# Performance work log

Hardware: AMD Instinct MI355X
Metric: run time of the kernel (lower is better)

The kernel has to match this reference:

```python
import jax, jax.numpy as jnp
import numpy as np

B, S, DIM = 2, 2048, 2048
N_HEADS, N_KV_HEADS = 16, 4
HEAD_DIM = DIM // N_HEADS  # 128
N_REP = N_HEADS // N_KV_HEADS  # 4
ROPE_THETA = 10000.0


def setup_inputs() -> dict:
    key = jax.random.key(0)
    ks = jax.random.split(key, 6)
    x = jax.random.normal(ks[0], (B, S, DIM), dtype=jnp.float32)
    # torch nn.Linear weights are [out_features, in_features]
    sc = 0.02
    wq = jax.random.normal(ks[1], (N_HEADS * HEAD_DIM, DIM), dtype=jnp.float32) * sc
    wk = jax.random.normal(ks[2], (N_KV_HEADS * HEAD_DIM, DIM), dtype=jnp.float32) * sc
    wv = jax.random.normal(ks[3], (N_KV_HEADS * HEAD_DIM, DIM), dtype=jnp.float32) * sc
    wo = jax.random.normal(ks[4], (DIM, N_HEADS * HEAD_DIM), dtype=jnp.float32) * sc
    # precomputed rotary table (freqs_cis in llama): [S, head_dim//2]
    inv_freq = 1.0 / (ROPE_THETA ** (jnp.arange(0, HEAD_DIM, 2, dtype=jnp.float32) / HEAD_DIM))
    t = jnp.arange(S, dtype=jnp.float32)
    freqs = jnp.outer(t, inv_freq)  # [S, head_dim//2]
    freqs_cos = jnp.cos(freqs)
    freqs_sin = jnp.sin(freqs)
    # additive causal mask as passed to SDPA (float, 0 on allowed, -inf-like elsewhere)
    causal = jnp.tril(jnp.ones((S, S), dtype=bool))
    mask = jnp.where(causal, 0.0, -1e9).astype(jnp.float32)
    return {"x": x, "wq": wq, "wk": wk, "wv": wv, "wo": wo,
            "freqs_cos": freqs_cos, "freqs_sin": freqs_sin, "mask": mask}


def _apply_rope(t, cos, sin):
    # t: [B, S, H, D]; cos/sin: [S, D//2] -> complex multiply on adjacent pairs
    tr = t.reshape(*t.shape[:-1], -1, 2)  # [B,S,H,D/2,2]
    tre, tim = tr[..., 0], tr[..., 1]
    c = cos[None, :, None, :]
    s = sin[None, :, None, :]
    out_re = tre * c - tim * s
    out_im = tre * s + tim * c
    return jnp.stack([out_re, out_im], axis=-1).reshape(t.shape)


def reference(x, wq, wk, wv, wo, freqs_cos, freqs_sin, mask):
    Bx, Sx, _ = x.shape
    xq = (x @ wq.T).reshape(Bx, Sx, N_HEADS, HEAD_DIM)
    xk = (x @ wk.T).reshape(Bx, Sx, N_KV_HEADS, HEAD_DIM)
    xv = (x @ wv.T).reshape(Bx, Sx, N_KV_HEADS, HEAD_DIM)
    xq = _apply_rope(xq, freqs_cos, freqs_sin)
    xk = _apply_rope(xk, freqs_cos, freqs_sin)
    # repeat_kv for GQA: [B,S,KV,D] -> [B,S,KV*n_rep,D]
    keys = jnp.repeat(xk, N_REP, axis=2)
    values = jnp.repeat(xv, N_REP, axis=2)
    q = xq.transpose(0, 2, 1, 3)      # [B,H,S,D]
    k = keys.transpose(0, 2, 1, 3)
    v = values.transpose(0, 2, 1, 3)
    scale = 1.0 / jnp.sqrt(jnp.float32(HEAD_DIM))
    scores = jnp.einsum('bhqd,bhkd->bhqk', q, k) * scale + mask[None, None]
    attn = jax.nn.softmax(scores, axis=-1)
    out = jnp.einsum('bhqk,bhkd->bhqd', attn, v)
    out = out.transpose(0, 2, 1, 3).reshape(Bx, Sx, -1)
    return out @ wo.T
```

## Files before the change

kernel.cpp:

```cpp
#include <hip/hip_runtime.h>
#include <hip/hip_bf16.h>

#define B_   2
#define S_   2048
#define DIM_ 2048
#define NH   16
#define NKV  4
#define HD   128
#define QKVN 3072

typedef __attribute__((ext_vector_type(8)))  short  sv8;
typedef __attribute__((ext_vector_type(8)))  ushort usv8;
typedef __attribute__((ext_vector_type(4)))  float  fv4;
typedef __attribute__((ext_vector_type(16))) float  fv16;

__device__ __forceinline__ float fast_exp2(float x) {
  return __builtin_amdgcn_exp2f(x);
}

__device__ __forceinline__ ushort f2bf(float f) {
  __hip_bfloat16 h = __float2bfloat16(f);
  union { __hip_bfloat16 h; ushort u; } c; c.h = h; return c.u;
}
__device__ __forceinline__ float bf2f(ushort u) {
  union { unsigned int i; float f; } c; c.i = ((unsigned)u) << 16; return c.f;
}

__device__ __forceinline__ unsigned int cvtpk(float lo, float hi) {
  unsigned int r;
  asm("v_cvt_pk_bf16_f32 %0, %1, %2" : "=v"(r) : "v"(lo), "v"(hi));
  return r;
}
__device__ __forceinline__ unsigned int xhalf(unsigned int x) {
  return (unsigned int)__shfl_xor((int)x, 32, 64);
}

__device__ __forceinline__ float tmax16(const fv16& v) {
  float a = fmaxf(fmaxf(v[0], v[1]),  fmaxf(v[2], v[3]));
  float b = fmaxf(fmaxf(v[4], v[5]),  fmaxf(v[6], v[7]));
  float c = fmaxf(fmaxf(v[8], v[9]),  fmaxf(v[10], v[11]));
  float d = fmaxf(fmaxf(v[12], v[13]), fmaxf(v[14], v[15]));
  return fmaxf(fmaxf(a, b), fmaxf(c, d));
}
__device__ __forceinline__ float tsum16(const fv16& v) {
  float a = (v[0] + v[1]) + (v[2] + v[3]);
  float b = (v[4] + v[5]) + (v[6] + v[7]);
  float c = (v[8] + v[9]) + (v[10] + v[11]);
  float d = (v[12] + v[13]) + (v[14] + v[15]);
  return (a + b) + (c + d);
}

__device__ __forceinline__ void async16(const void* g, void* l) {
  __builtin_amdgcn_global_load_lds(
      (const __attribute__((address_space(1))) unsigned int*)g,
      (__attribute__((address_space(3))) unsigned int*)l, 16, 0, 0);
}

__global__ void cvtall_kernel(const float* __restrict__ x,
                              const float* __restrict__ wq, const float* __restrict__ wk,
                              const float* __restrict__ wv, const float* __restrict__ wo,
                              const float* __restrict__ fc, const float* __restrict__ fs,
                              ushort* __restrict__ xb,
                              ushort* __restrict__ wqkvb, ushort* __restrict__ wob,
                              float* __restrict__ cs2) {
  const int NX = 2 * 2048 * 2048;
  const int NQ = 2048 * 2048, NK = 512 * 2048;
  const int CVT = NX + 2 * NQ + 2 * NK;
  int i = (blockIdx.x * 256 + threadIdx.x) * 4;
  if (i < CVT) {
    const float* src; ushort* dst;
    if (i < NX) { src = x + i; dst = xb + i; }
    else {
      int j = i - NX;
      if (j < NQ)               { src = wq + j;             dst = wqkvb + j; }
      else if (j < NQ + NK)     { src = wk + (j - NQ);      dst = wqkvb + j; }
      else if (j < NQ + 2 * NK) { src = wv + (j - NQ - NK); dst = wqkvb + j; }
      else                      { int k = j - (NQ + 2 * NK); src = wo + k; dst = wob + k; }
    }
    fv4 v = *(const fv4*)src;
    ushort4 o;
    o.x = f2bf(v[0]); o.y = f2bf(v[1]); o.z = f2bf(v[2]); o.w = f2bf(v[3]);
    *(ushort4*)dst = o;
  } else {
    int j = i - CVT;
    fv4 c = *(const fv4*)(fc + j);
    fv4 s = *(const fv4*)(fs + j);
    fv4 lo, hi;
    lo[0] = c[0]; lo[1] = s[0]; lo[2] = c[1]; lo[3] = s[1];
    hi[0] = c[2]; hi[1] = s[2]; hi[2] = c[3]; hi[3] = s[3];
    *(fv4*)(cs2 + 2 * j)     = lo;
    *(fv4*)(cs2 + 2 * j + 4) = hi;
  }
}

__global__ __launch_bounds__(256) void vtrans_kernel(const ushort* __restrict__ vraw,
                                                     ushort* __restrict__ vt, int rowstride) {
  __shared__ ushort tile[128][136];
  int blk = blockIdx.x;
  int st  = blk & 15;
  int kvb = blk >> 4;
  int kv  = kvb & 3;
  int b   = kvb >> 2;
  int s0  = st << 7;
#pragma unroll
  for (int it = 0; it < 8; ++it) {
    int t = it * 256 + threadIdx.x;
    int srow = t >> 4;
    int d8 = (t & 15) * 8;
    usv8 v = *(const usv8*)(vraw + (size_t)(b * S_ + s0 + srow) * rowstride + kv * HD + d8);
#pragma unroll
    for (int j = 0; j < 8; ++j) tile[d8 + j][srow] = v[j];
  }
  __syncthreads();
#pragma unroll
  for (int it = 0; it < 8; ++it) {
    int t = it * 256 + threadIdx.x;
    int d = t >> 4;
    int s8 = (t & 15) * 8;
    usv8 o;
#pragma unroll
    for (int j = 0; j < 8; ++j) o[j] = tile[d][s8 + j];
    *(usv8*)(vt + ((size_t)(b * NKV + kv) * HD + d) * S_ + s0 + s8) = o;
  }
}

__global__ __launch_bounds__(512) void gemm192_rope(const ushort* __restrict__ A,
                                                    const ushort* __restrict__ Bm,
                                                    const float* __restrict__ cs2,
                                                    ushort* __restrict__ qr,
                                                    ushort* __restrict__ kr,
                                                    ushort* __restrict__ Cv,
                                                    float qscale,
                                                    int M, int N, int K) {
  __shared__ __align__(16) ushort SM[57344];
  int nb = N / 192;
  int bx = blockIdx.x % nb, by = blockIdx.x / nb;
  int m0 = by << 8;
  int n0 = bx * 192;
  int tid = threadIdx.x;
  int lane = tid & 63, w = tid >> 6;
  int l15 = lane & 15, lg = lane >> 4;
  int wm = (w >> 2) * 128;
  int wn = (w & 3) * 48;
  int pA = w >> 2;

  int srow = tid >> 3;
  int cb   = ((tid & 7) * 16) ^ ((srow & 7) << 4);
  const ushort* sA = A  + (size_t)(m0 + srow) * K + (cb >> 1);
  const ushort* sB = Bm + (size_t)(n0 + srow) * K + (cb >> 1);
  size_t rstep = (size_t)64 * K;
  int nkt = K >> 6;

  auto STG_A = [&](int t, int db) {
    ushort* base = SM + db * 28672 + (w << 9);
    const ushort* a0 = sA + (size_t)t * 64;
    async16(a0,             base);
    async16(a0 + rstep,     base + 4096);
    async16(a0 + 2 * rstep, base + 8192);
    async16(a0 + 3 * rstep, base + 12288);
  };
  auto STG_B = [&](int t, int db) {
    ushort* base = SM + db * 28672 + 16384 + (w << 9);
    const ushort* b0 = sB + (size_t)t * 64;
    async16(b0,             base);
    async16(b0 + rstep,     base + 4096);
    async16(b0 + 2 * rstep, base + 8192);
  };

  fv4 acc[8][3] = {};
  sv8 alo[4][2], ahi[4][2], b01[2][2], b2v[2];

  STG_A(0, 0); STG_B(0, 0);
  { int t1 = nkt > 1 ? 1 : 0; STG_A(t1, 1); STG_B(t1, 1); }
  asm volatile("s_waitcnt vmcnt(7)");
  __builtin_amdgcn_s_barrier();

  for (int t = 0; t < nkt; ++t) {
    int db = t & 1;
    int t2 = t + 2 < nkt ? t + 2 : nkt - 1;
    const char* Ab = (const char*)(SM + db * 28672) + pA * 16384;
    const char* Bb = (const char*)(SM + db * 28672) + 32768;

#pragma unroll
    for (int m = 0; m < 4; ++m)
#pragma unroll
      for (int kk = 0; kk < 2; ++kk) {
        int row = m * 16 + l15;
        alo[m][kk] = *(const sv8*)(Ab + row * 128 + ((kk * 64 + lg * 16) ^ ((row & 7) << 4)));
      }
#pragma unroll
    for (int j = 0; j < 2; ++j)
#pragma unroll
      for (int kk = 0; kk < 2; ++kk) {
        int row = wn + j * 16 + l15;
        b01[j][kk] = *(const sv8*)(Bb + row * 128 + ((kk * 64 + lg * 16) ^ ((row & 7) << 4)));
      }
    __builtin_amdgcn_s_barrier();
    asm volatile("s_waitcnt lgkmcnt(0)");
    __builtin_amdgcn_s_setprio(1);
#pragma unroll
    for (int m = 0; m < 4; ++m)
#pragma unroll
      for (int j = 0; j < 2; ++j)
#pragma unroll
        for (int kk = 0; kk < 2; ++kk)
          acc[m][j] = __builtin_amdgcn_mfma_f32_16x16x32_bf16(alo[m][kk], b01[j][kk], acc[m][j], 0, 0, 0);
    __builtin_amdgcn_s_setprio(0);
    __builtin_amdgcn_s_barrier();

#pragma unroll
    for (int m = 0; m < 4; ++m)
#pragma unroll
      for (int kk = 0; kk < 2; ++kk) {
        int row = 64 + m * 16 + l15;
        ahi[m][kk] = *(const sv8*)(Ab + row * 128 + ((kk * 64 + lg * 16) ^ ((row & 7) << 4)));
      }
#pragma unroll
    for (int kk = 0; kk < 2; ++kk) {
      int row = wn + 32 + l15;
      b2v[kk] = *(const sv8*)(Bb + row * 128 + ((kk * 64 + lg * 16) ^ ((row & 7) << 4)));
    }
    __builtin_amdgcn_s_barrier();
    asm volatile("s_waitcnt lgkmcnt(0)");
    __builtin_amdgcn_s_setprio(1);
#pragma unroll
    for (int m = 0; m < 4; ++m)
#pragma unroll
      for (int kk = 0; kk < 2; ++kk)
        acc[m][2] = __builtin_amdgcn_mfma_f32_16x16x32_bf16(alo[m][kk], b2v[kk], acc[m][2], 0, 0, 0);
    __builtin_amdgcn_s_setprio(0);
    __builtin_amdgcn_s_barrier();

    STG_A(t2, db);
    __builtin_amdgcn_s_barrier();
    __builtin_amdgcn_s_setprio(1);
#pragma unroll
    for (int m = 0; m < 4; ++m)
#pragma unroll
      for (int j = 0; j < 2; ++j)
#pragma unroll
        for (int kk = 0; kk < 2; ++kk)
          acc[m + 4][j] = __builtin_amdgcn_mfma_f32_16x16x32_bf16(ahi[m][kk], b01[j][kk], acc[m + 4][j], 0, 0, 0);
    __builtin_amdgcn_s_setprio(0);
    __builtin_amdgcn_s_barrier();

    STG_B(t2, db);
    asm volatile("s_waitcnt vmcnt(7)");
    __builtin_amdgcn_s_barrier();
    __builtin_amdgcn_s_setprio(1);
#pragma unroll
    for (int m = 0; m < 4; ++m)
#pragma unroll
      for (int kk = 0; kk < 2; ++kk)
        acc[m + 4][2] = __builtin_amdgcn_mfma_f32_16x16x32_bf16(ahi[m][kk], b2v[kk], acc[m + 4][2], 0, 0, 0);
    __builtin_amdgcn_s_setprio(0);
    __builtin_amdgcn_s_barrier();
  }

  asm volatile("s_waitcnt vmcnt(0)");
  int lpar = lane & 1;
#pragma unroll
  for (int m = 0; m < 8; ++m)
#pragma unroll
    for (int j = 0; j < 3; ++j) {
      int col = n0 + wn + j * 16 + l15;
      if (col >= 2560) {
#pragma unroll
        for (int r = 0; r < 4; ++r) {
          int row = m0 + wm + m * 16 + lg * 4 + r;
          Cv[(size_t)row * QKVN + col] = f2bf(acc[m][j][r]);
        }
      } else {
        bool isQ  = col < 2048;
        int hcol  = isQ ? col : col - 2048;
        int hidx  = hcol >> 7;
        int d     = col & 127;
        int dp    = d >> 1;
        float scale = isQ ? qscale : 1.0f;
        ushort* base = isQ ? qr : kr;
        int heads = isQ ? NH : NKV;
#pragma unroll
        for (int r = 0; r < 4; ++r) {
          int row = m0 + wm + m * 16 + lg * 4 + r;
          int s   = row & (S_ - 1);
          int bb  = row >> 11;
          float val = acc[m][j][r];
          float pv  = __shfl_xor(val, 1, 64);
          float2 cs = *(const float2*)(cs2 + 2 * (s * 64 + dp));
          float outv = (lpar ? (pv * cs.y + val * cs.x) : (val * cs.x - pv * cs.y)) * scale;
          base[((size_t)(bb * heads + hidx) * S_ + s) * HD + d] = f2bf(outv);
        }
      }
    }
}

template <typename OutT>
__global__ __launch_bounds__(512) void gemmOP(const ushort* __restrict__ A,
                                              const ushort* __restrict__ Bm,
                                              OutT* __restrict__ C,
                                              int M, int N, int K) {
  __shared__ __align__(16) ushort SM[49152];
  int nb = N >> 7;
  int bx = blockIdx.x % nb, by = blockIdx.x / nb;
  int m0 = by << 8, n0 = bx << 7;
  int tid = threadIdx.x;
  int lane = tid & 63, w = tid >> 6;
  int l15 = lane & 15, lg = lane >> 4;
  int wm = (w >> 2) * 128;
  int wn = (w & 3) * 32;
  int pA = (w >> 2);

  int srow = tid >> 3;
  int cb   = ((tid & 7) * 16) ^ ((srow & 7) << 4);
  const ushort* sA0 = A  + (size_t)(m0 + srow) * K + (cb >> 1);
  const ushort* sB0 = Bm + (size_t)(n0 + srow) * K + (cb >> 1);
  const ushort* srcs[3] = { sA0, sA0 + (size_t)128 * K, sB0 };
  size_t rstep = (size_t)64 * K;

  int nkt = K >> 6;

  auto STG = [&](int part, int t, int db) {
    ushort* d0 = SM + db * 24576 + part * 8192 + (w << 9);
    const ushort* s0 = srcs[part] + t * 64;
    async16(s0, d0);
    async16(s0 + rstep, d0 + 4096);
  };

  fv4 acc[8][2] = {};
  sv8 a[8][2], b[2][2];

#pragma unroll
  for (int p = 0; p < 3; ++p) STG(p, 0, 0);
  {
    int t1 = 1 < nkt ? 1 : 0;
#pragma unroll
    for (int p = 0; p < 3; ++p) STG(p, t1, 1);
  }
  asm volatile("s_waitcnt vmcnt(6)");
  __builtin_amdgcn_s_barrier();

  for (int t = 0; t < nkt; ++t) {
    int db = t & 1;
    int t2 = t + 2 < nkt ? t + 2 : nkt - 1;
    const char* Ab = (const char*)SM + db * 49152 + pA * 16384;
    const char* Bb = (const char*)SM + db * 49152 + 32768;

#pragma unroll
    for (int m = 0; m < 8; ++m)
#pragma unroll
      for (int kk = 0; kk < 2; ++kk) {
        int row = m * 16 + l15;
        a[m][kk] = *(const sv8*)(Ab + row * 128 + ((kk * 64 + lg * 16) ^ ((row & 7) << 4)));
      }
#pragma unroll
    for (int j = 0; j < 2; ++j)
#pragma unroll
      for (int kk = 0; kk < 2; ++kk) {
        int row = wn + j * 16 + l15;
        b[j][kk] = *(const sv8*)(Bb + row * 128 + ((kk * 64 + lg * 16) ^ ((row & 7) << 4)));
      }
    __builtin_amdgcn_s_barrier();
    asm volatile("s_waitcnt lgkmcnt(0)");
    __builtin_amdgcn_s_setprio(1);
#pragma unroll
    for (int m = 0; m < 4; ++m)
#pragma unroll
      for (int j = 0; j < 2; ++j)
#pragma unroll
        for (int kk = 0; kk < 2; ++kk)
          acc[m][j] = __builtin_amdgcn_mfma_f32_16x16x32_bf16(a[m][kk], b[j][kk], acc[m][j], 0, 0, 0);
    __builtin_amdgcn_s_setprio(0);
    __builtin_amdgcn_s_barrier();

    STG(0, t2, db);
    STG(1, t2, db);
    STG(2, t2, db);
    asm volatile("s_waitcnt vmcnt(6)");
    __builtin_amdgcn_s_barrier();
    __builtin_amdgcn_s_setprio(1);
#pragma unroll
    for (int m = 0; m < 4; ++m)
#pragma unroll
      for (int j = 0; j < 2; ++j)
#pragma unroll
        for (int kk = 0; kk < 2; ++kk)
          acc[m + 4][j] = __builtin_amdgcn_mfma_f32_16x16x32_bf16(a[m + 4][kk], b[j][kk], acc[m + 4][j], 0, 0, 0);
    __builtin_amdgcn_s_setprio(0);
    __builtin_amdgcn_s_barrier();
  }

  asm volatile("s_waitcnt vmcnt(0)");
#pragma unroll
  for (int m = 0; m < 8; ++m)
#pragma unroll
    for (int j = 0; j < 2; ++j)
#pragma unroll
      for (int r = 0; r < 4; ++r) {
        int row = m0 + wm + m * 16 + lg * 4 + r;
        int col = n0 + wn + j * 16 + l15;
        if constexpr (sizeof(OutT) == 2) C[(size_t)row * N + col] = (OutT)f2bf(acc[m][j][r]);
        else                             C[(size_t)row * N + col] = (OutT)acc[m][j][r];
      }
}

__global__ __launch_bounds__(512, 2) void attn_kernel(const ushort* __restrict__ Q,
                                                      const ushort* __restrict__ Kr,
                                                      const ushort* __restrict__ Vt,
                                                      ushort* __restrict__ O) {
  __shared__ __align__(16) ushort SMEM[65536];

  int blk = blockIdx.x;
  int bh  = blk & 31;
  int pr  = blk >> 5;
  int h   = bh & 15;
  int b   = bh >> 4;
  int kv  = h >> 2;
  int lane = threadIdx.x & 63, w = threadIdx.x >> 6;
  int wg = w & 3, Hf = w >> 2;
  int l31 = lane & 31, hh = lane >> 5;

  const ushort* Qbase = Q  + (size_t)(b * NH  + h ) * S_ * HD;
  const ushort* Kbase = Kr + (size_t)(b * NKV + kv) * S_ * HD;
  const ushort* Vbase = Vt + (size_t)(b * NKV + kv) * HD * S_;

  const ushort* kSrc[4]; ushort* kDst[2][4];
  const ushort* vSrc[4]; ushort* vDst[2][4];
#pragma unroll
  for (int it = 0; it < 4; ++it) {
    int lin = it * 4096 + wg * 1024 + lane * 16;
    { int row = lin >> 8; int cbv = (lin & 255) ^ ((row & 15) << 4);
      kSrc[it] = Kbase + (size_t)row * HD + (cbv >> 1); }
    { int row = lin >> 8; int cp = lin & 255; int cl = cp ^ ((row & 15) << 4);
      int d = row + ((cl >> 7) << 6);
      int koff = (cl & 127) >> 1;
      vSrc[it] = Vbase + (size_t)d * S_ + koff; }
#pragma unroll
    for (int buf = 0; buf < 2; ++buf) {
      kDst[buf][it] = SMEM + Hf * 16384 + buf * 8192 + ((it * 4096 + wg * 1024) >> 1);
      vDst[buf][it] = SMEM + 32768 + Hf * 16384 + buf * 8192 + ((it * 4096 + wg * 1024) >> 1);
    }
  }

  float* cML = (float*)SMEM;
  float* cO  = (float*)SMEM + 512;

  for (int pass = 0; pass < 2; ++pass) {
    int qt = pass ? (15 - pr) : pr;
    int q0 = qt << 7;
    int qrow_w = q0 + wg * 32;
    int myq    = qrow_w + l31;
    int nj     = qt + 1;
    int ktbase = Hf * nj;

    sv8 qf[8];
#pragma unroll
    for (int kk = 0; kk < 8; ++kk)
      qf[kk] = *(const sv8*)(Qbase + (size_t)myq * HD + kk * 16 + hh * 8);

    fv16 oacc[4] = {};
    float mrun = -1e30f, lrun = 0.f;

    {
      size_t k0 = (size_t)ktbase << 6;
#pragma unroll
      for (int it = 0; it < 4; ++it) async16(kSrc[it] + k0 * HD, kDst[0][it]);
#pragma unroll
      for (int it = 0; it < 4; ++it) async16(vSrc[it] + k0,      vDst[0][it]);
    }

    for (int j = 0; j < nj; ++j) {
      int cur = j & 1, nxt = cur ^ 1;
      __syncthreads();
      if (j + 1 < nj) {
        size_t k0n = (size_t)(ktbase + j + 1) << 6;
#pragma unroll
        for (int it = 0; it < 4; ++it) async16(kSrc[it] + k0n * HD, kDst[nxt][it]);
#pragma unroll
        for (int it = 0; it < 4; ++it) async16(vSrc[it] + k0n,      vDst[nxt][it]);
      }
      const char* KsC = (const char*)(SMEM + Hf * 16384 + cur * 8192);
      const char* VsC = (const char*)(SMEM + 32768 + Hf * 16384 + cur * 8192);
      int k0 = (ktbase + j) << 6;

      fv16 sacc[2] = {};
      __builtin_amdgcn_s_setprio(1);
#pragma unroll
      for (int kk = 0; kk < 8; ++kk) {
        int cbq = kk * 32 + hh * 16;
        int r0 = l31, r1 = 32 + l31;
        sv8 kf0 = *(const sv8*)(KsC + r0 * 256 + (cbq ^ ((r0 & 15) << 4)));
        sv8 kf1 = *(const sv8*)(KsC + r1 * 256 + (cbq ^ ((r1 & 15) << 4)));
        sacc[0] = __builtin_amdgcn_mfma_f32_32x32x16_bf16(kf0, qf[kk], sacc[0], 0, 0, 0);
        sacc[1] = __builtin_amdgcn_mfma_f32_32x32x16_bf16(kf1, qf[kk], sacc[1], 0, 0, 0);
      }
      __builtin_amdgcn_s_setprio(0);

      if (k0 + 63 > qrow_w) {
        int thr = myq - k0 - 4 * hh;
#pragma unroll
        for (int t = 0; t < 2; ++t)
#pragma unroll
          for (int r = 0; r < 16; ++r) {
            int kp = t * 32 + (r & 3) + 8 * (r >> 2);
            if (kp > thr) sacc[t][r] = -1e38f;
          }
      }

      float tmax = fmaxf(tmax16(sacc[0]), tmax16(sacc[1]));
      tmax = fmaxf(tmax, __shfl_xor(tmax, 32, 64));

      if (__any(tmax > mrun + 8.0f)) {
        float mnew = fmaxf(mrun, tmax);
        float esc  = fast_exp2(mrun - mnew);
        lrun *= esc;
        float er[16];
#pragma unroll
        for (int r = 0; r < 16; ++r) er[r] = __shfl(esc, (r & 3) + 8 * (r >> 2) + 4 * hh, 64);
#pragma unroll
        for (int d0 = 0; d0 < 4; ++d0)
#pragma unroll
          for (int r = 0; r < 16; ++r) oacc[d0][r] *= er[r];
        mrun = mnew;
      }

#pragma unroll
      for (int t = 0; t < 2; ++t)
#pragma unroll
        for (int r = 0; r < 16; ++r) sacc[t][r] = fast_exp2(sacc[t][r] - mrun);
      float psum = tsum16(sacc[0]) + tsum16(sacc[1]);
      psum += __shfl_xor(psum, 32, 64);
      lrun += psum;

      union Frag { unsigned int u[4]; sv8 v; } pa[4];
#pragma unroll
      for (int t = 0; t < 2; ++t)
#pragma unroll
        for (int half = 0; half < 2; ++half) {
          int cbq = half * 8;
          unsigned int a0 = cvtpk(sacc[t][cbq + 0], sacc[t][cbq + 1]);
          unsigned int a1 = cvtpk(sacc[t][cbq + 2], sacc[t][cbq + 3]);
          unsigned int b0 = cvtpk(sacc[t][cbq + 4], sacc[t][cbq + 5]);
          unsigned int b1 = cvtpk(sacc[t][cbq + 6], sacc[t][cbq + 7]);
          unsigned int a0p = xhalf(a0), a1p = xhalf(a1);
          unsigned int b0p = xhalf(b0), b1p = xhalf(b1);
          pa[2 * t + half].u[0] = hh ? b0p : a0;
          pa[2 * t + half].u[1] = hh ? b1p : a1;
          pa[2 * t + half].u[2] = hh ? b0  : a0p;
          pa[2 * t + half].u[3] = hh ? b1  : a1p;
        }

      __builtin_amdgcn_s_setprio(1);
#pragma unroll
      for (int ks = 0; ks < 4; ++ks) {
#pragma unroll
        for (int d0 = 0; d0 < 4; ++d0) {
          int d = d0 * 32 + l31;
          int row = d & 63;
          int cl = ((d >> 6) << 7) + ks * 32 + hh * 16;
          sv8 vf = *(const sv8*)(VsC + row * 256 + (cl ^ ((row & 15) << 4)));
          oacc[d0] = __builtin_amdgcn_mfma_f32_32x32x16_bf16(pa[ks].v, vf, oacc[d0], 0, 0, 0);
        }
      }
      __builtin_amdgcn_s_setprio(0);
    }

    __syncthreads();
    if (Hf) {
      int base = wg * 64 + lane;
      cML[base * 2]     = mrun;
      cML[base * 2 + 1] = lrun;
      float* dst = cO + base * 65;
#pragma unroll
      for (int d0 = 0; d0 < 4; ++d0)
#pragma unroll
        for (int r = 0; r < 16; ++r) dst[d0 * 16 + r] = oacc[d0][r];
    }
    __syncthreads();
    if (!Hf) {
      int base = wg * 64 + lane;
      float m2 = cML[base * 2], l2 = cML[base * 2 + 1];
      const float* src = cO + base * 65;
      float m  = fmaxf(mrun, m2);
      float e1 = fast_exp2(mrun - m), e2 = fast_exp2(m2 - m);
      float l  = lrun * e1 + l2 * e2;
      float inv = 1.0f / l;
      float f1 = e1 * inv, f2 = e2 * inv;
      float f1b[16], f2b[16];
#pragma unroll
      for (int r = 0; r < 16; ++r) {
        int ro = (r & 3) + 8 * (r >> 2) + 4 * hh;
        f1b[r] = __shfl(f1, ro, 64);
        f2b[r] = __shfl(f2, ro, 64);
      }
#pragma unroll
      for (int r = 0; r < 16; ++r) {
        int q = qrow_w + (r & 3) + 8 * (r >> 2) + 4 * hh;
#pragma unroll
        for (int d0 = 0; d0 < 4; ++d0) {
          int d = d0 * 32 + l31;
          float val = oacc[d0][r] * f1b[r] + src[d0 * 16 + r] * f2b[r];
          O[(size_t)(b * S_ + q) * DIM_ + h * HD + d] = f2bf(val);
        }
      }
    }
    __syncthreads();
  }
}

extern "C" void kernel_launch(void* const* d_in, const int* in_sizes, int n_in,
                              void* d_out, int out_size, void* d_ws, size_t ws_size,
                              hipStream_t stream) {
  const float* x  = (const float*)d_in[0];
  const float* wq = (const float*)d_in[1];
  const float* wk = (const float*)d_in[2];
  const float* wv = (const float*)d_in[3];
  const float* wo = (const float*)d_in[4];
  const float* fc = (const float*)d_in[5];
  const float* fs = (const float*)d_in[6];
  float* out = (float*)d_out;

  char* ws = (char*)d_ws;
  size_t off = 0;
  auto alloc = [&](size_t bytes) -> ushort* {
    ushort* p = (ushort*)(ws + off);
    off += (bytes + 255) & ~(size_t)255;
    return p;
  };
  ushort* xb    = alloc((size_t)B_ * S_ * DIM_ * 2);
  ushort* wqkvb = alloc((size_t)QKVN * DIM_ * 2);
  ushort* wob   = alloc((size_t)DIM_ * DIM_ * 2);
  ushort* qkvr  = alloc((size_t)B_ * S_ * QKVN * 2);
  ushort* qr    = alloc((size_t)B_ * S_ * DIM_ * 2);
  ushort* kr    = alloc((size_t)B_ * S_ * NKV * HD * 2);
  ushort* vtb   = alloc((size_t)B_ * S_ * NKV * HD * 2);
  ushort* obf   = alloc((size_t)B_ * S_ * DIM_ * 2);
  float*  cs2   = (float*)alloc((size_t)S_ * 64 * 2 * 4);
  (void)ws_size; (void)n_in; (void)in_sizes; (void)out_size;

  const int cvt_elems = 2 * DIM_ * DIM_  + 2 * DIM_ * DIM_
                      + 2 * NKV * HD * DIM_ ;
  const int total_elems = cvt_elems + S_ * 64 ;
  cvtall_kernel<<<total_elems / 1024, 256, 0, stream>>>(x, wq, wk, wv, wo, fc, fs,
                                                        xb, wqkvb, wob, cs2);

  const float qscale = 0.08838834764831845f * 1.4426950408889634f;
  gemm192_rope<<<(B_ * S_ / 256) * (QKVN / 192), 512, 0, stream>>>(
      xb, wqkvb, cs2, qr, kr, qkvr, qscale, B_ * S_, QKVN, DIM_);

  vtrans_kernel<<<B_ * NKV * (S_ / 128), 256, 0, stream>>>(qkvr + 2560, vtb, QKVN);

  attn_kernel<<<B_ * NH * 8, 512, 0, stream>>>(qr, kr, vtb, obf);

  gemmOP<float><<<(B_ * S_ / 256) * (DIM_ / 128), 512, 0, stream>>>(obf, wob, out, B_ * S_, DIM_, DIM_);
}
```

Measured before the change: 179.2 us.

## Single-buffer attention K/V tiles, one q-tile per block, raise occupancy

Result: slower. 262.2 us (+46.3%).

```diff
diff --git a/kernel.cpp b/kernel.cpp
--- a/kernel.cpp
+++ b/kernel.cpp
@@ -403,28 +403,34 @@
       }
 }
 
-__global__ __launch_bounds__(512, 2) void attn_kernel(const ushort* __restrict__ Q,
+__global__ __launch_bounds__(512, 4) void attn_kernel(const ushort* __restrict__ Q,
                                                       const ushort* __restrict__ Kr,
                                                       const ushort* __restrict__ Vt,
                                                       ushort* __restrict__ O) {
-  __shared__ __align__(16) ushort SMEM[65536];
+  __shared__ __align__(16) ushort SMEM[34304];
 
   int blk = blockIdx.x;
-  int bh  = blk & 31;
-  int pr  = blk >> 5;
+  int bh, qt;
+  if (blk < 256) { bh = blk & 31; qt = 15 - (blk >> 5); }
+  else           { int c = blk - 256; bh = c & 31; qt = c >> 5; }
   int h   = bh & 15;
   int b   = bh >> 4;
   int kv  = h >> 2;
   int lane = threadIdx.x & 63, w = threadIdx.x >> 6;
   int wg = w & 3, Hf = w >> 2;
   int l31 = lane & 31, hh = lane >> 5;
+  int q0 = qt << 7;
+  int qrow_w = q0 + wg * 32;
+  int myq    = qrow_w + l31;
+  int nj     = qt + 1;
+  int ktbase = Hf * nj;
 
   const ushort* Qbase = Q  + (size_t)(b * NH  + h ) * S_ * HD;
   const ushort* Kbase = Kr + (size_t)(b * NKV + kv) * S_ * HD;
   const ushort* Vbase = Vt + (size_t)(b * NKV + kv) * HD * S_;
 
-  const ushort* kSrc[4]; ushort* kDst[2][4];
-  const ushort* vSrc[4]; ushort* vDst[2][4];
+  const ushort* kSrc[4]; ushort* kDst[4];
+  const ushort* vSrc[4]; ushort* vDst[4];
 #pragma unroll
   for (int it = 0; it < 4; ++it) {
     int lin = it * 4096 + wg * 1024 + lane * 16;
@@ -434,176 +440,155 @@
       int d = row + ((cl >> 7) << 6);
       int koff = (cl & 127) >> 1;
       vSrc[it] = Vbase + (size_t)d * S_ + koff; }
-#pragma unroll
-    for (int buf = 0; buf < 2; ++buf) {
-      kDst[buf][it] = SMEM + Hf * 16384 + buf * 8192 + ((it * 4096 + wg * 1024) >> 1);
-      vDst[buf][it] = SMEM + 32768 + Hf * 16384 + buf * 8192 + ((it * 4096 + wg * 1024) >> 1);
-    }
+    kDst[it] = SMEM + Hf * 8192 + ((it * 4096 + wg * 1024) >> 1);
+    vDst[it] = SMEM + 16384 + Hf * 8192 + ((it * 4096 + wg * 1024) >> 1);
+  }
+
+  sv8 qf[8];
+#pragma unroll
+  for (int kk = 0; kk < 8; ++kk)
+    qf[kk] = *(const sv8*)(Qbase + (size_t)myq * HD + kk * 16 + hh * 8);
+
+  fv16 oacc[4] = {};
+  float mrun = -1e30f, lrun = 0.f;
+
+  const char* KsC = (const char*)(SMEM + Hf * 8192);
+  const char* VsC = (const char*)(SMEM + 16384 + Hf * 8192);
+
+  for (int j = 0; j < nj; ++j) {
+    if (j) __syncthreads();
+    {
+      size_t k0g = (size_t)(ktbase + j) << 6;
+#pragma unroll
+      for (int it = 0; it < 4; ++it) async16(kSrc[it] + k0g * HD, kDst[it]);
+#pragma unroll
+      for (int it = 0; it < 4; ++it) async16(vSrc[it] + k0g,      vDst[it]);
+    }
+    __syncthreads();
+    int k0 = (ktbase + j) << 6;
+
+    fv16 sacc[2] = {};
+    __builtin_amdgcn_s_setprio(1);
+#pragma unroll
+    for (int kk = 0; kk < 8; ++kk) {
+      int cbq = kk * 32 + hh * 16;
+      int r0 = l31, r1 = 32 + l31;
+      sv8 kf0 = *(const sv8*)(KsC + r0 * 256 + (cbq ^ ((r0 & 15) << 4)));
+      sv8 kf1 = *(const sv8*)(KsC + r1 * 256 + (cbq ^ ((r1 & 15) << 4)));
+      sacc[0] = __builtin_amdgcn_mfma_f32_32x32x16_bf16(kf0, qf[kk], sacc[0], 0, 0, 0);
+      sacc[1] = __builtin_amdgcn_mfma_f32_32x32x16_bf16(kf1, qf[kk], sacc[1], 0, 0, 0);
+    }
+    __builtin_amdgcn_s_setprio(0);
+
+    if (k0 + 63 > qrow_w) {
+      int thr = myq - k0 - 4 * hh;
+#pragma unroll
+      for (int t = 0; t < 2; ++t)
+#pragma unroll
+        for (int r = 0; r < 16; ++r) {
+          int kp = t * 32 + (r & 3) + 8 * (r >> 2);
+          if (kp > thr) sacc[t][r] = -1e38f;
+        }
+    }
+
+    float tmax = fmaxf(tmax16(sacc[0]), tmax16(sacc[1]));
+    tmax = fmaxf(tmax, __shfl_xor(tmax, 32, 64));
+
+    if (__any(tmax > mrun + 8.0f)) {
+      float mnew = fmaxf(mrun, tmax);
+      float esc  = fast_exp2(mrun - mnew);
+      lrun *= esc;
+      float er[16];
+#pragma unroll
+      for (int r = 0; r < 16; ++r) er[r] = __shfl(esc, (r & 3) + 8 * (r >> 2) + 4 * hh, 64);
+#pragma unroll
+      for (int d0 = 0; d0 < 4; ++d0)
+#pragma unroll
+        for (int r = 0; r < 16; ++r) oacc[d0][r] *= er[r];
+      mrun = mnew;
+    }
+
+#pragma unroll
+    for (int t = 0; t < 2; ++t)
+#pragma unroll
+      for (int r = 0; r < 16; ++r) sacc[t][r] = fast_exp2(sacc[t][r] - mrun);
+    float psum = tsum16(sacc[0]) + tsum16(sacc[1]);
+    psum += __shfl_xor(psum, 32, 64);
+    lrun += psum;
+
+    union Frag { unsigned int u[4]; sv8 v; } pa[4];
+#pragma unroll
+    for (int t = 0; t < 2; ++t)
+#pragma unroll
+      for (int half = 0; half < 2; ++half) {
+        int cbq = half * 8;
+        unsigned int a0 = cvtpk(sacc[t][cbq + 0], sacc[t][cbq + 1]);
+        unsigned int a1 = cvtpk(sacc[t][cbq + 2], sacc[t][cbq + 3]);
+        unsigned int b0 = cvtpk(sacc[t][cbq + 4], sacc[t][cbq + 5]);
+        unsigned int b1 = cvtpk(sacc[t][cbq + 6], sacc[t][cbq + 7]);
+        unsigned int a0p = xhalf(a0), a1p = xhalf(a1);
+        unsigned int b0p = xhalf(b0), b1p = xhalf(b1);
+        pa[2 * t + half].u[0] = hh ? b0p : a0;
+        pa[2 * t + half].u[1] = hh ? b1p : a1;
+        pa[2 * t + half].u[2] = hh ? b0  : a0p;
+        pa[2 * t + half].u[3] = hh ? b1  : a1p;
+      }
+
+    __builtin_amdgcn_s_setprio(1);
+#pragma unroll
+    for (int ks = 0; ks < 4; ++ks) {
+#pragma unroll
+      for (int d0 = 0; d0 < 4; ++d0) {
+        int d = d0 * 32 + l31;
+        int row = d & 63;
+        int cl = ((d >> 6) << 7) + ks * 32 + hh * 16;
+        sv8 vf = *(const sv8*)(VsC + row * 256 + (cl ^ ((row & 15) << 4)));
+        oacc[d0] = __builtin_amdgcn_mfma_f32_32x32x16_bf16(pa[ks].v, vf, oacc[d0], 0, 0, 0);
+      }
+    }
+    __builtin_amdgcn_s_setprio(0);
   }
 
   float* cML = (float*)SMEM;
   float* cO  = (float*)SMEM + 512;
-
-  for (int pass = 0; pass < 2; ++pass) {
-    int qt = pass ? (15 - pr) : pr;
-    int q0 = qt << 7;
-    int qrow_w = q0 + wg * 32;
-    int myq    = qrow_w + l31;
-    int nj     = qt + 1;
-    int ktbase = Hf * nj;
-
-    sv8 qf[8];
-#pragma unroll
-    for (int kk = 0; kk < 8; ++kk)
-      qf[kk] = *(const sv8*)(Qbase + (size_t)myq * HD + kk * 16 + hh * 8);
-
-    fv16 oacc[4] = {};
-    float mrun = -1e30f, lrun = 0.f;
-
-    {
-      size_t k0 = (size_t)ktbase << 6;
-#pragma unroll
-      for (int it = 0; it < 4; ++it) async16(kSrc[it] + k0 * HD, kDst[0][it]);
-#pragma unroll
-      for (int it = 0; it < 4; ++it) async16(vSrc[it] + k0,      vDst[0][it]);
-    }
-
-    for (int j = 0; j < nj; ++j) {
-      int cur = j & 1, nxt = cur ^ 1;
-      __syncthreads();
-      if (j + 1 < nj) {
-        size_t k0n = (size_t)(ktbase + j + 1) << 6;
-#pragma unroll
-        for (int it = 0; it < 4; ++it) async16(kSrc[it] + k0n * HD, kDst[nxt][it]);
-#pragma unroll
-        for (int it = 0; it < 4; ++it) async16(vSrc[it] + k0n,      vDst[nxt][it]);
-      }
-      const char* KsC = (const char*)(SMEM + Hf * 16384 + cur * 8192);
-      const char* VsC = (const char*)(SMEM + 32768 + Hf * 16384 + cur * 8192);
-      int k0 = (ktbase + j) << 6;
-
-      fv16 sacc[2] = {};
-      __builtin_amdgcn_s_setprio(1);
-#pragma unroll
-      for (int kk = 0; kk < 8; ++kk) {
-        int cbq = kk * 32 + hh * 16;
-        int r0 = l31, r1 = 32 + l31;
-        sv8 kf0 = *(const sv8*)(KsC + r0 * 256 + (cbq ^ ((r0 & 15) << 4)));
-        sv8 kf1 = *(const sv8*)(KsC + r1 * 256 + (cbq ^ ((r1 & 15) << 4)));
-        sacc[0] = __builtin_amdgcn_mfma_f32_32x32x16_bf16(kf0, qf[kk], sacc[0], 0, 0, 0);
-        sacc[1] = __builtin_amdgcn_mfma_f32_32x32x16_bf16(kf1, qf[kk], sacc[1], 0, 0, 0);
-      }
-      __builtin_amdgcn_s_setprio(0);
-
-      if (k0 + 63 > qrow_w) {
-        int thr = myq - k0 - 4 * hh;
-#pragma unroll
-        for (int t = 0; t < 2; ++t)
-#pragma unroll
-          for (int r = 0; r < 16; ++r) {
-            int kp = t * 32 + (r & 3) + 8 * (r >> 2);
-            if (kp > thr) sacc[t][r] = -1e38f;
-          }
-      }
-
-      float tmax = fmaxf(tmax16(sacc[0]), tmax16(sacc[1]));
-      tmax = fmaxf(tmax, __shfl_xor(tmax, 32, 64));
-
-      if (__any(tmax > mrun + 8.0f)) {
-        float mnew = fmaxf(mrun, tmax);
-        float esc  = fast_exp2(mrun - mnew);
-        lrun *= esc;
-        float er[16];
-#pragma unroll
-        for (int r = 0; r < 16; ++r) er[r] = __shfl(esc, (r & 3) + 8 * (r >> 2) + 4 * hh, 64);
-#pragma unroll
-        for (int d0 = 0; d0 < 4; ++d0)
-#pragma unroll
-          for (int r = 0; r < 16; ++r) oacc[d0][r] *= er[r];
-        mrun = mnew;
-      }
-
-#pragma unroll
-      for (int t = 0; t < 2; ++t)
-#pragma unroll
-        for (int r = 0; r < 16; ++r) sacc[t][r] = fast_exp2(sacc[t][r] - mrun);
-      float psum = tsum16(sacc[0]) + tsum16(sacc[1]);
-      psum += __shfl_xor(psum, 32, 64);
-      lrun += psum;
-
-      union Frag { unsigned int u[4]; sv8 v; } pa[4];
-#pragma unroll
-      for (int t = 0; t < 2; ++t)
-#pragma unroll
-        for (int half = 0; half < 2; ++half) {
-          int cbq = half * 8;
-          unsigned int a0 = cvtpk(sacc[t][cbq + 0], sacc[t][cbq + 1]);
-          unsigned int a1 = cvtpk(sacc[t][cbq + 2], sacc[t][cbq + 3]);
-          unsigned int b0 = cvtpk(sacc[t][cbq + 4], sacc[t][cbq + 5]);
-          unsigned int b1 = cvtpk(sacc[t][cbq + 6], sacc[t][cbq + 7]);
-          unsigned int a0p = xhalf(a0), a1p = xhalf(a1);
-          unsigned int b0p = xhalf(b0), b1p = xhalf(b1);
-          pa[2 * t + half].u[0] = hh ? b0p : a0;
-          pa[2 * t + half].u[1] = hh ? b1p : a1;
-          pa[2 * t + half].u[2] = hh ? b0  : a0p;
-          pa[2 * t + half].u[3] = hh ? b1  : a1p;
-        }
-
-      __builtin_amdgcn_s_setprio(1);
-#pragma unroll
-      for (int ks = 0; ks < 4; ++ks) {
-#pragma unroll
-        for (int d0 = 0; d0 < 4; ++d0) {
-          int d = d0 * 32 + l31;
-          int row = d & 63;
-          int cl = ((d >> 6) << 7) + ks * 32 + hh * 16;
-          sv8 vf = *(const sv8*)(VsC + row * 256 + (cl ^ ((row & 15) << 4)));
-          oacc[d0] = __builtin_amdgcn_mfma_f32_32x32x16_bf16(pa[ks].v, vf, oacc[d0], 0, 0, 0);
-        }
-      }
-      __builtin_amdgcn_s_setprio(0);
-    }
-
-    __syncthreads();
-    if (Hf) {
-      int base = wg * 64 + lane;
-      cML[base * 2]     = mrun;
-      cML[base * 2 + 1] = lrun;
-      float* dst = cO + base * 65;
-#pragma unroll
-      for (int d0 = 0; d0 < 4; ++d0)
-#pragma unroll
-        for (int r = 0; r < 16; ++r) dst[d0 * 16 + r] = oacc[d0][r];
-    }
-    __syncthreads();
-    if (!Hf) {
-      int base = wg * 64 + lane;
-      float m2 = cML[base * 2], l2 = cML[base * 2 + 1];
-      const float* src = cO + base * 65;
-      float m  = fmaxf(mrun, m2);
-      float e1 = fast_exp2(mrun - m), e2 = fast_exp2(m2 - m);
-      float l  = lrun * e1 + l2 * e2;
-      float inv = 1.0f / l;
-      float f1 = e1 * inv, f2 = e2 * inv;
-      float f1b[16], f2b[16];
-#pragma unroll
-      for (int r = 0; r < 16; ++r) {
-        int ro = (r & 3) + 8 * (r >> 2) + 4 * hh;
-        f1b[r] = __shfl(f1, ro, 64);
-        f2b[r] = __shfl(f2, ro, 64);
-      }
-#pragma unroll
-      for (int r = 0; r < 16; ++r) {
-        int q = qrow_w + (r & 3) + 8 * (r >> 2) + 4 * hh;
-#pragma unroll
-        for (int d0 = 0; d0 < 4; ++d0) {
-          int d = d0 * 32 + l31;
-          float val = oacc[d0][r] * f1b[r] + src[d0 * 16 + r] * f2b[r];
-          O[(size_t)(b * S_ + q) * DIM_ + h * HD + d] = f2bf(val);
-        }
-      }
-    }
-    __syncthreads();
+  __syncthreads();
+  if (Hf) {
+    int base = wg * 64 + lane;
+    cML[base * 2]     = mrun;
+    cML[base * 2 + 1] = lrun;
+    float* dst = cO + base * 65;
+#pragma unroll
+    for (int d0 = 0; d0 < 4; ++d0)
+#pragma unroll
+      for (int r = 0; r < 16; ++r) dst[d0 * 16 + r] = oacc[d0][r];
+  }
+  __syncthreads();
+  if (!Hf) {
+    int base = wg * 64 + lane;
+    float m2 = cML[base * 2], l2 = cML[base * 2 + 1];
+    const float* src = cO + base * 65;
+    float m  = fmaxf(mrun, m2);
+    float e1 = fast_exp2(mrun - m), e2 = fast_exp2(m2 - m);
+    float l  = lrun * e1 + l2 * e2;
+    float inv = 1.0f / l;
+    float f1 = e1 * inv, f2 = e2 * inv;
+    float f1b[16], f2b[16];
+#pragma unroll
+    for (int r = 0; r < 16; ++r) {
+      int ro = (r & 3) + 8 * (r >> 2) + 4 * hh;
+      f1b[r] = __shfl(f1, ro, 64);
+      f2b[r] = __shfl(f2, ro, 64);
+    }
+#pragma unroll
+    for (int r = 0; r < 16; ++r) {
+      int q = qrow_w + (r & 3) + 8 * (r >> 2) + 4 * hh;
+#pragma unroll
+      for (int d0 = 0; d0 < 4; ++d0) {
+        int d = d0 * 32 + l31;
+        float val = oacc[d0][r] * f1b[r] + src[d0 * 16 + r] * f2b[r];
+        O[(size_t)(b * S_ + q) * DIM_ + h * HD + d] = f2bf(val);
+      }
+    }
   }
 }
 
@@ -649,7 +634,7 @@
 
   vtrans_kernel<<<B_ * NKV * (S_ / 128), 256, 0, stream>>>(qkvr + 2560, vtb, QKVN);
 
-  attn_kernel<<<B_ * NH * 8, 512, 0, stream>>>(qr, kr, vtb, obf);
+  attn_kernel<<<512, 512, 0, stream>>>(qr, kr, vtb, obf);
 
   gemmOP<float><<<(B_ * S_ / 256) * (DIM_ / 128), 512, 0, stream>>>(obf, wob, out, B_ * S_, DIM_, DIM_);
 }
```
